# Kernel tuning notes

Measured on AMD Instinct MI355X. Metric: run time of the kernel, lower is better.

## Reference

```python
import jax, jax.numpy as jnp
import numpy as np

N_LAYER = 4
N_HEAD = 8
N_EMBD = 512
HEAD_SIZE = N_EMBD // N_HEAD
VOCAB = 32000
BLOCK = 2048
WINDOW = 64
N_GLOBAL = 16
N_RANDOM = 16
B = 2
T = 2048


def setup_inputs() -> dict:
    key = jax.random.key(0)
    ks = jax.random.split(key, 24)
    s = 0.02
    inp = {
        "tok_emb": jax.random.normal(ks[0], (VOCAB, N_EMBD), jnp.float32) * s,
        "pos_emb": jax.random.normal(ks[1], (BLOCK, N_EMBD), jnp.float32) * s,
        "Wq": jax.random.normal(ks[2], (N_LAYER, N_HEAD, N_EMBD, HEAD_SIZE), jnp.float32) * s,
        "Wk": jax.random.normal(ks[3], (N_LAYER, N_HEAD, N_EMBD, HEAD_SIZE), jnp.float32) * s,
        "Wv": jax.random.normal(ks[4], (N_LAYER, N_HEAD, N_EMBD, HEAD_SIZE), jnp.float32) * s,
        "Wproj": jax.random.normal(ks[5], (N_LAYER, N_EMBD, N_EMBD), jnp.float32) * s,
        "bproj": jnp.zeros((N_LAYER, N_EMBD), jnp.float32),
        "ln1_g": jnp.ones((N_LAYER, N_EMBD), jnp.float32),
        "ln1_b": jnp.zeros((N_LAYER, N_EMBD), jnp.float32),
        "ln2_g": jnp.ones((N_LAYER, N_EMBD), jnp.float32),
        "ln2_b": jnp.zeros((N_LAYER, N_EMBD), jnp.float32),
        "W1": jax.random.normal(ks[6], (N_LAYER, N_EMBD, 4 * N_EMBD), jnp.float32) * s,
        "b1": jnp.zeros((N_LAYER, 4 * N_EMBD), jnp.float32),
        "W2": jax.random.normal(ks[7], (N_LAYER, 4 * N_EMBD, N_EMBD), jnp.float32) * s,
        "b2": jnp.zeros((N_LAYER, N_EMBD), jnp.float32),
        "lnf_g": jnp.ones((N_EMBD,), jnp.float32),
        "lnf_b": jnp.zeros((N_EMBD,), jnp.float32),
        "Wout": jax.random.normal(ks[8], (N_EMBD, VOCAB), jnp.float32) * s,
        "bout": jnp.zeros((VOCAB,), jnp.float32),
        "input_tokens": jax.random.randint(ks[9], (B, T), 0, VOCAB, jnp.int32),
        "random_cols": jax.random.randint(ks[10], (N_LAYER, N_HEAD, T, N_RANDOM), 0, T, jnp.int32),
    }
    return inp


def _layernorm(x, g, b):
    mu = jnp.mean(x, axis=-1, keepdims=True)
    var = jnp.var(x, axis=-1, keepdims=True)
    return (x - mu) * jax.lax.rsqrt(var + 1e-5) * g + b


def _static_masks(t):
    rows = jnp.arange(t)[:, None]
    cols = jnp.arange(t)[None, :]
    causal = rows >= cols
    local = (cols >= rows - WINDOW + 1) & (cols <= rows)
    glob = (rows < N_GLOBAL) | (cols < N_GLOBAL)
    return local | glob, causal  # base [T,T], causal [T,T]


def _random_mask(rc):  # rc: [H, T, R] -> [H, T, T] bool
    h, t, r = rc.shape
    m = jnp.zeros((h, t, t), dtype=bool)
    hi = jnp.arange(h)[:, None, None]
    ri = jnp.arange(t)[None, :, None]
    return m.at[hi, ri, rc].set(True)


def _forward(tok_emb, pos_emb, Wq, Wk, Wv, Wproj, bproj, ln1_g, ln1_b, ln2_g, ln2_b,
             W1, b1, W2, b2, lnf_g, lnf_b, Wout, bout, input_tokens, random_cols):
    b, t = input_tokens.shape
    x = tok_emb[input_tokens] + pos_emb[:t]  # [B,T,C]
    base, causal = _static_masks(t)
    scale = HEAD_SIZE ** -0.5
    neg_inf = jnp.finfo(x.dtype).min
    for l in range(N_LAYER):
        xn = _layernorm(x, ln1_g[l], ln1_b[l])
        q = jnp.einsum('btc,hcd->bhtd', xn, Wq[l])
        k = jnp.einsum('btc,hcd->bhtd', xn, Wk[l])
        v = jnp.einsum('btc,hcd->bhtd', xn, Wv[l])
        w = jnp.einsum('bhtd,bhsd->bhts', q, k) * scale  # [B,H,T,T]
        final = (base[None] | _random_mask(random_cols[l])) & causal[None]  # [H,T,T]
        w = jnp.where(final[None], w, neg_inf)
        w = jax.nn.softmax(w, axis=-1)
        attn = jnp.einsum('bhts,bhsd->bhtd', w, v)  # [B,H,T,hs]
        attn = attn.transpose(0, 2, 1, 3).reshape(b, t, N_EMBD)
        x = x + attn @ Wproj[l] + bproj[l]
        xn = _layernorm(x, ln2_g[l], ln2_b[l])
        h = jax.nn.relu(xn @ W1[l] + b1[l])
        x = x + h @ W2[l] + b2[l]
    x = _layernorm(x, lnf_g, lnf_b)
    return x @ Wout + bout  # logits [B,T,V]


def reference(tok_emb, pos_emb, Wq, Wk, Wv, Wproj, bproj, ln1_g, ln1_b, ln2_g, ln2_b,
              W1, b1, W2, b2, lnf_g, lnf_b, Wout, bout, input_tokens, random_cols):
    return _forward(tok_emb, pos_emb, Wq, Wk, Wv, Wproj, bproj, ln1_g, ln1_b, ln2_g, ln2_b,
                    W1, b1, W2, b2, lnf_g, lnf_b, Wout, bout, input_tokens, random_cols)
```

## Files before the change

kernel.cpp:

```cpp
#include <hip/hip_runtime.h>
#include <hip/hip_bf16.h>

#define NLAYER 4
#define NHEAD 8
#define CEMB 512
#define HS 64
#define VOCAB_N 32000
#define SEQT 2048
#define BATCH_N 2
#define MROWS (BATCH_N * SEQT)
#define WIN 64
#define NGLOB 16
#define NRAND 16
#define QB 16

typedef __attribute__((ext_vector_type(8))) __bf16 bf16x8;
typedef __attribute__((ext_vector_type(4))) float f32x4;
typedef __attribute__((ext_vector_type(8))) unsigned short u16x8;

__device__ __forceinline__ unsigned short f2bf(float f) {
    unsigned u = __float_as_uint(f);
    u += 0x7fffu + ((u >> 16) & 1u);
    return (unsigned short)(u >> 16);
}
__device__ __forceinline__ float bf2f(unsigned short v) {
    return __uint_as_float((unsigned)v << 16);
}

__device__ __forceinline__ void stage16(const unsigned short* g, unsigned short* l) {
    __builtin_amdgcn_global_load_lds(
        (const __attribute__((address_space(1))) void*)g,
        (__attribute__((address_space(3))) void*)l, 16, 0, 0);
}

__global__ __launch_bounds__(256) void transpose_all_kernel(
    const float* __restrict__ Wq, const float* __restrict__ Wk,
    const float* __restrict__ Wv, const float* __restrict__ Wproj,
    const float* __restrict__ W1, const float* __restrict__ W2,
    const float* __restrict__ Wout,
    unsigned short* __restrict__ wqkvT, unsigned short* __restrict__ wprojT,
    unsigned short* __restrict__ w1T, unsigned short* __restrict__ w2T,
    unsigned short* __restrict__ woutT)
{
    __shared__ float tle[64][65];
    const int bid = blockIdx.x;
    const float* src; unsigned short* dst; int Ks, Ns, k0, n0;
    if (bid < 768) {
        const int tile = bid & 7, rest = bid >> 3;
        const int l = rest / 24, r2 = rest % 24;
        const int sel = r2 >> 3, h = r2 & 7;
        const float* W = (sel == 0) ? Wq : (sel == 1) ? Wk : Wv;
        src = W + (size_t)(l * 8 + h) * 512 * 64;
        dst = wqkvT + ((size_t)l * 1536 + sel * 512 + h * 64) * 512;
        Ks = 512; Ns = 64; k0 = tile * 64; n0 = 0;
    } else if (bid < 1024) {
        const int idx = bid - 768, l = idx >> 6, t6 = idx & 63;
        src = Wproj + (size_t)l * 512 * 512;
        dst = wprojT + (size_t)l * 512 * 512;
        Ks = 512; Ns = 512; k0 = (t6 >> 3) * 64; n0 = (t6 & 7) * 64;
    } else if (bid < 2048) {
        const int idx = bid - 1024, l = idx >> 8, t8 = idx & 255;
        src = W1 + (size_t)l * 512 * 2048;
        dst = w1T + (size_t)l * 2048 * 512;
        Ks = 512; Ns = 2048; k0 = (t8 >> 5) * 64; n0 = (t8 & 31) * 64;
    } else if (bid < 3072) {
        const int idx = bid - 2048, l = idx >> 8, t8 = idx & 255;
        src = W2 + (size_t)l * 2048 * 512;
        dst = w2T + (size_t)l * 512 * 2048;
        Ks = 2048; Ns = 512; k0 = (t8 >> 3) * 64; n0 = (t8 & 7) * 64;
    } else {
        const int idx = bid - 3072;
        src = Wout; dst = woutT;
        Ks = 512; Ns = 32000; k0 = (idx / 500) * 64; n0 = (idx % 500) * 64;
    }
    const int tid = threadIdx.x;
    #pragma unroll
    for (int i = 0; i < 16; ++i) {
        const int idx = tid + i * 256;
        const int r = idx >> 6, c = idx & 63;
        tle[r][c] = src[(size_t)(k0 + r) * Ns + n0 + c];
    }
    __syncthreads();
    #pragma unroll
    for (int i = 0; i < 16; ++i) {
        const int idx = tid + i * 256;
        const int c = idx >> 6, r = idx & 63;
        dst[(size_t)(n0 + c) * Ks + k0 + r] = f2bf(tle[r][c]);
    }
}

__global__ __launch_bounds__(256) void embed_kernel(
    const float* __restrict__ tok_emb, const float* __restrict__ pos_emb,
    const int* __restrict__ toks, float* __restrict__ x)
{
    int i = blockIdx.x * 256 + threadIdx.x;
    int m = i >> 7;
    int c = (i & 127) << 2;
    int tok = toks[m];
    const float4 a = *(const float4*)&tok_emb[(size_t)tok * CEMB + c];
    const float4 p = *(const float4*)&pos_emb[(size_t)(m & (SEQT - 1)) * CEMB + c];
    float4 o;
    o.x = a.x + p.x; o.y = a.y + p.y; o.z = a.z + p.z; o.w = a.w + p.w;
    *(float4*)&x[(size_t)m * CEMB + c] = o;
}

__global__ __launch_bounds__(256) void ln_kernel(
    const float* __restrict__ x, const float* __restrict__ g,
    const float* __restrict__ b, unsigned short* __restrict__ out)
{
    const int wave = threadIdx.x >> 6, lane = threadIdx.x & 63;
    const int m = blockIdx.x * 4 + wave;
    const float* row = x + (size_t)m * CEMB;
    const float4 v0 = *(const float4*)&row[lane * 8];
    const float4 v1 = *(const float4*)&row[lane * 8 + 4];
    float s  = v0.x + v0.y + v0.z + v0.w + v1.x + v1.y + v1.z + v1.w;
    float s2 = v0.x*v0.x + v0.y*v0.y + v0.z*v0.z + v0.w*v0.w
             + v1.x*v1.x + v1.y*v1.y + v1.z*v1.z + v1.w*v1.w;
    #pragma unroll
    for (int off = 32; off > 0; off >>= 1) {
        s  += __shfl_xor(s, off);
        s2 += __shfl_xor(s2, off);
    }
    const float mu  = s * (1.f / CEMB);
    const float var = s2 * (1.f / CEMB) - mu * mu;
    const float rs  = rsqrtf(var + 1e-5f);
    const float vals[8] = {v0.x, v0.y, v0.z, v0.w, v1.x, v1.y, v1.z, v1.w};
    u16x8 o;
    #pragma unroll
    for (int j = 0; j < 8; ++j)
        o[j] = f2bf((vals[j] - mu) * rs * g[lane * 8 + j] + b[lane * 8 + j]);
    *(u16x8*)&out[(size_t)m * CEMB + lane * 8] = o;
}

template<int MODE, int NF, int SWZ>
__global__ __launch_bounds__(256) void gemm_kernel(
    const unsigned short* __restrict__ A, const unsigned short* __restrict__ Bt,
    const float* __restrict__ bias, const float* resid, void* outp,
    int M, int N, int K)
{
    __shared__ unsigned short sa[2][128 * 32];
    __shared__ unsigned short sb[2][NF * 32 * 32];
    const int tid = threadIdx.x;
    const int lane = tid & 63;
    const int wave = tid >> 6;
    const int wr = wave >> 1, wc = wave & 1;

    int bx = blockIdx.x, by = blockIdx.y;
    if (SWZ == 2) {
        const int flat = by * gridDim.x + bx;
        const int q = (gridDim.x * gridDim.y) >> 3;
        const int nl = (flat & 7) * q + (flat >> 3);
        by = nl & 31;
        bx = nl >> 5;
    }
    const int m0 = by * 128;
    const int n0 = bx * (NF * 32);

    const int c0a = (wave * 2) * 64 + lane;
    const int c1a = (wave * 2 + 1) * 64 + lane;
    const int r0 = c0a >> 2, kk0 = (c0a & 3) * 8;
    const int r1 = c1a >> 2, kk1 = (c1a & 3) * 8;
    const unsigned short* ga0 = A + (size_t)(m0 + r0) * K + kk0;
    const unsigned short* ga1 = A + (size_t)(m0 + r1) * K + kk1;
    const int o0 = (wave * 2) * 512;
    const int o1 = (wave * 2 + 1) * 512;
    const int cb0 = (NF == 4) ? c0a : wave * 64 + lane;
    const int cb1 = c1a;
    const int rb0 = cb0 >> 2, kb0 = (cb0 & 3) * 8;
    const int rb1 = cb1 >> 2, kb1 = (cb1 & 3) * 8;
    const unsigned short* gb0 = Bt + (size_t)(n0 + rb0) * K + kb0;
    const unsigned short* gb1 = Bt + (size_t)(n0 + rb1) * K + kb1;
    const int ob0 = (NF == 4) ? o0 : wave * 512;
    const int ob1 = o1;

    f32x4 acc[4][NF] = {};
    const int kro = (lane >> 4) * 8;
    const int fr = lane & 15;

    stage16(ga0, &sa[0][o0]);
    stage16(ga1, &sa[0][o1]);
    stage16(gb0, &sb[0][ob0]);
    if (NF == 4) stage16(gb1, &sb[0][ob1]);
    __syncthreads();

    const int nt = K >> 5;
    int cur = 0;
    for (int t = 0; t < nt; ++t) {
        if (t + 1 < nt) {
            const int k1 = (t + 1) << 5;
            stage16(ga0 + k1, &sa[cur ^ 1][o0]);
            stage16(ga1 + k1, &sa[cur ^ 1][o1]);
            stage16(gb0 + k1, &sb[cur ^ 1][ob0]);
            if (NF == 4) stage16(gb1 + k1, &sb[cur ^ 1][ob1]);
        }
        bf16x8 af[4], bfr[NF];
        #pragma unroll
        for (int i = 0; i < 4; ++i)
            af[i] = *reinterpret_cast<const bf16x8*>(&sa[cur][(wr * 64 + i * 16 + fr) * 32 + kro]);
        #pragma unroll
        for (int i = 0; i < NF; ++i)
            bfr[i] = *reinterpret_cast<const bf16x8*>(&sb[cur][(wc * (NF * 16) + i * 16 + fr) * 32 + kro]);
        #pragma unroll
        for (int mi = 0; mi < 4; ++mi)
            #pragma unroll
            for (int ni = 0; ni < NF; ++ni)
                acc[mi][ni] = __builtin_amdgcn_mfma_f32_16x16x32_bf16(af[mi], bfr[ni], acc[mi][ni], 0, 0, 0);
        __syncthreads();
        cur ^= 1;
    }

    #pragma unroll
    for (int mi = 0; mi < 4; ++mi) {
        #pragma unroll
        for (int ni = 0; ni < NF; ++ni) {
            const int gc = n0 + wc * (NF * 16) + ni * 16 + fr;
            const float bv = (MODE != 0) ? bias[gc] : 0.f;
            #pragma unroll
            for (int r = 0; r < 4; ++r) {
                const int gr = m0 + wr * 64 + mi * 16 + (lane >> 4) * 4 + r;
                float v = acc[mi][ni][r] + bv;
                if (MODE == 1) v += resid[(size_t)gr * N + gc];
                if (MODE == 2) v = fmaxf(v, 0.f);
                if (MODE == 0 || MODE == 2) {
                    ((unsigned short*)outp)[(size_t)gr * N + gc] = f2bf(v);
                } else {
                    ((float*)outp)[(size_t)gr * N + gc] = v;
                }
            }
        }
    }
}

__global__ __launch_bounds__(256) void attn_kernel(
    const unsigned short* __restrict__ qkv, const int* __restrict__ rc,
    unsigned short* __restrict__ attnout)
{
    __shared__ unsigned short Kw[80 * 64];
    __shared__ unsigned short Vw[80 * 64];
    __shared__ float ewA[4][64];
    __shared__ float cwW[4][40];
    __shared__ int   cwC[4][40];

    const int tid = threadIdx.x;
    const int wave = tid >> 6, lane = tid & 63;
    const int bid = blockIdx.x;
    const int tb = bid & 127;
    const int h = (bid >> 7) & 7;
    const int b = bid >> 10;
    const int t0 = tb * QB;
    const int base = t0 - 63;

    const unsigned short* kb = qkv + (size_t)b * SEQT * 1536 + 512 + h * 64;
    const unsigned short* vb = qkv + (size_t)b * SEQT * 1536 + 1024 + h * 64;

    for (int c = tid; c < 79 * 8; c += 256) {
        const int r = c >> 3, j = c & 7;
        const int col = base + r;
        u16x8 kv = {0, 0, 0, 0, 0, 0, 0, 0};
        u16x8 vv = {0, 0, 0, 0, 0, 0, 0, 0};
        if (col >= 0) {
            kv = *(const u16x8*)&kb[(size_t)col * 1536 + j * 8];
            vv = *(const u16x8*)&vb[(size_t)col * 1536 + j * 8];
        }
        *(u16x8*)&Kw[r * 64 + ((j ^ (r & 7)) * 8)] = kv;
        *(u16x8*)&Vw[r * 64 + j * 8] = vv;
    }
    __syncthreads();

    for (int u = 0; u < 4; ++u) {
        const int Q = wave * 4 + u;
        const int t = t0 + Q;
        const int m = b * SEQT + t;

        u16x8 qreg[8];
        #pragma unroll
        for (int j = 0; j < 8; ++j)
            qreg[j] = *(const u16x8*)&qkv[(size_t)m * 1536 + h * 64 + j * 8];

        const int row = Q + lane;
        const int colA = base + row;
        float sA;
        {
            float s = 0.f;
            #pragma unroll
            for (int j = 0; j < 8; ++j) {
                const u16x8 kc = *(const u16x8*)&Kw[row * 64 + ((j ^ (row & 7)) * 8)];
                #pragma unroll
                for (int e = 0; e < 8; ++e)
                    s += bf2f(kc[e]) * bf2f(qreg[j][e]);
            }
            sA = (colA >= NGLOB) ? s * 0.125f : -1e30f;
        }

        int colB = 0;
        bool vB = false;
        if (lane < NGLOB) {
            colB = lane;
            vB = (lane <= t);
        } else if (lane < 32) {
            colB = rc[((size_t)h * SEQT + t) * NRAND + (lane - 16)];
            vB = (colB >= NGLOB) && (colB <= t - WIN);
        }
        #pragma unroll
        for (int j = 0; j < 15; ++j) {
            const int cj = __shfl(colB, 16 + j);
            if (lane >= 16 && lane < 32 && (lane - 16) > j && cj == colB) vB = false;
        }

        float sB = -1e30f;
        if (vB) {
            float s = 0.f;
            const unsigned short* kr = &kb[(size_t)colB * 1536];
            #pragma unroll
            for (int j = 0; j < 8; ++j) {
                const u16x8 kc = *(const u16x8*)&kr[j * 8];
                #pragma unroll
                for (int e = 0; e < 8; ++e)
                    s += bf2f(kc[e]) * bf2f(qreg[j][e]);
            }
            sB = s * 0.125f;
        }

        float mx = fmaxf(sA, sB);
        #pragma unroll
        for (int off = 32; off > 0; off >>= 1) mx = fmaxf(mx, __shfl_xor(mx, off));
        const float e0 = (colA >= NGLOB) ? __expf(sA - mx) : 0.f;
        const float e1 = vB ? __expf(sB - mx) : 0.f;
        float sum = e0 + e1;
        #pragma unroll
        for (int off = 32; off > 0; off >>= 1) sum += __shfl_xor(sum, off);
        const float inv = 1.f / sum;

        ewA[wave][lane] = e0;
        const unsigned long long bm = __ballot(vB);
        const int nB = __popcll(bm);
        const int pos = __popcll(bm & ((1ull << lane) - 1ull));
        if (vB) { cwC[wave][pos] = colB; cwW[wave][pos] = e1; }
        if (lane >= 32 && lane < 36) {
            const int p = nB + (lane - 32);
            cwC[wave][p] = 0; cwW[wave][p] = 0.f;
        }

        float acc = 0.f;
        #pragma unroll 8
        for (int s = 0; s < 64; ++s)
            acc += ewA[wave][s] * bf2f(Vw[(Q + s) * 64 + lane]);

        const int nB4 = (nB + 3) & ~3;
        for (int i = 0; i < nB4; i += 4) {
            const float w0 = cwW[wave][i + 0], w1 = cwW[wave][i + 1];
            const float w2 = cwW[wave][i + 2], w3 = cwW[wave][i + 3];
            const int   c0 = cwC[wave][i + 0], c1 = cwC[wave][i + 1];
            const int   c2 = cwC[wave][i + 2], c3 = cwC[wave][i + 3];
            const float x0 = bf2f(vb[(size_t)c0 * 1536 + lane]);
            const float x1 = bf2f(vb[(size_t)c1 * 1536 + lane]);
            const float x2 = bf2f(vb[(size_t)c2 * 1536 + lane]);
            const float x3 = bf2f(vb[(size_t)c3 * 1536 + lane]);
            acc += w0 * x0 + w1 * x1 + w2 * x2 + w3 * x3;
        }

        attnout[(size_t)m * CEMB + h * 64 + lane] = f2bf(acc * inv);
    }
}

extern "C" void kernel_launch(void* const* d_in, const int* in_sizes, int n_in,
                              void* d_out, int out_size, void* d_ws, size_t ws_size,
                              hipStream_t stream)
{
    const float* tok_emb = (const float*)d_in[0];
    const float* pos_emb = (const float*)d_in[1];
    const float* Wq    = (const float*)d_in[2];
    const float* Wk    = (const float*)d_in[3];
    const float* Wv    = (const float*)d_in[4];
    const float* Wproj = (const float*)d_in[5];
    const float* bproj = (const float*)d_in[6];
    const float* ln1g  = (const float*)d_in[7];
    const float* ln1b  = (const float*)d_in[8];
    const float* ln2g  = (const float*)d_in[9];
    const float* ln2b  = (const float*)d_in[10];
    const float* W1    = (const float*)d_in[11];
    const float* b1    = (const float*)d_in[12];
    const float* W2    = (const float*)d_in[13];
    const float* b2    = (const float*)d_in[14];
    const float* lnfg  = (const float*)d_in[15];
    const float* lnfb  = (const float*)d_in[16];
    const float* Wout  = (const float*)d_in[17];
    const float* bout  = (const float*)d_in[18];
    const int*   toks  = (const int*)d_in[19];
    const int*   rcols = (const int*)d_in[20];
    (void)in_sizes; (void)n_in; (void)out_size; (void)ws_size;

    char* ws = (char*)d_ws;
    size_t off = 0;
    auto ALLOC = [&](size_t bytes) -> void* {
        void* p = ws + off;
        off += (bytes + 255) & ~(size_t)255;
        return p;
    };
    float*          x      = (float*)ALLOC((size_t)MROWS * CEMB * 4);
    unsigned short* xnbf   = (unsigned short*)ALLOC((size_t)MROWS * CEMB * 2);
    unsigned short* qkv    = (unsigned short*)ALLOC((size_t)MROWS * 1536 * 2);
    unsigned short* attnbf = (unsigned short*)ALLOC((size_t)MROWS * CEMB * 2);
    unsigned short* hbf    = (unsigned short*)ALLOC((size_t)MROWS * 2048 * 2);
    unsigned short* wqkvT  = (unsigned short*)ALLOC((size_t)NLAYER * 1536 * 512 * 2);
    unsigned short* wprojT = (unsigned short*)ALLOC((size_t)NLAYER * 512 * 512 * 2);
    unsigned short* w1T    = (unsigned short*)ALLOC((size_t)NLAYER * 2048 * 512 * 2);
    unsigned short* w2T    = (unsigned short*)ALLOC((size_t)NLAYER * 512 * 2048 * 2);
    unsigned short* woutT  = (unsigned short*)ALLOC((size_t)VOCAB_N * 512 * 2);

    transpose_all_kernel<<<7072, 256, 0, stream>>>(
        Wq, Wk, Wv, Wproj, W1, W2, Wout, wqkvT, wprojT, w1T, w2T, woutT);

    embed_kernel<<<2048, 256, 0, stream>>>(tok_emb, pos_emb, toks, x);

    for (int l = 0; l < NLAYER; ++l) {
        ln_kernel<<<1024, 256, 0, stream>>>(x, ln1g + l * CEMB, ln1b + l * CEMB, xnbf);
        gemm_kernel<0, 2, 0><<<dim3(24, 32), 256, 0, stream>>>(
            xnbf, wqkvT + (size_t)l * 1536 * 512, nullptr, nullptr, qkv, MROWS, 1536, 512);
        attn_kernel<<<2048, 256, 0, stream>>>(qkv, rcols + (size_t)l * NHEAD * SEQT * NRAND, attnbf);
        gemm_kernel<1, 2, 0><<<dim3(8, 32), 256, 0, stream>>>(
            attnbf, wprojT + (size_t)l * 512 * 512, bproj + l * CEMB, x, x, MROWS, 512, 512);
        ln_kernel<<<1024, 256, 0, stream>>>(x, ln2g + l * CEMB, ln2b + l * CEMB, xnbf);
        gemm_kernel<2, 4, 0><<<dim3(16, 32), 256, 0, stream>>>(
            xnbf, w1T + (size_t)l * 2048 * 512, b1 + l * 2048, nullptr, hbf, MROWS, 2048, 512);
        gemm_kernel<1, 2, 0><<<dim3(8, 32), 256, 0, stream>>>(
            hbf, w2T + (size_t)l * 512 * 2048, b2 + l * CEMB, x, x, MROWS, 512, 2048);
    }
    ln_kernel<<<1024, 256, 0, stream>>>(x, lnfg, lnfb, xnbf);
    gemm_kernel<3, 4, 2><<<dim3(250, 32), 256, 0, stream>>>(
        xnbf, woutT, bout, nullptr, d_out, MROWS, VOCAB_N, 512);
}
```

Baseline: 1.037 ms.

## Triple-buffer GEMM shared-memory staging with explicit vmcnt waits

New measurement: 1.035 ms. About the same (-0.2%).

```diff
diff --git a/kernel.cpp b/kernel.cpp
--- a/kernel.cpp
+++ b/kernel.cpp
@@ -138,8 +138,8 @@
     const float* __restrict__ bias, const float* resid, void* outp,
     int M, int N, int K)
 {
-    __shared__ unsigned short sa[2][128 * 32];
-    __shared__ unsigned short sb[2][NF * 32 * 32];
+    __shared__ unsigned short sa[3][128 * 32];
+    __shared__ unsigned short sb[3][NF * 32 * 32];
     const int tid = threadIdx.x;
     const int lane = tid & 63;
     const int wave = tid >> 6;
@@ -177,22 +177,34 @@
     const int kro = (lane >> 4) * 8;
     const int fr = lane & 15;
 
-    stage16(ga0, &sa[0][o0]);
-    stage16(ga1, &sa[0][o1]);
-    stage16(gb0, &sb[0][ob0]);
-    if (NF == 4) stage16(gb1, &sb[0][ob1]);
-    __syncthreads();
+    auto STAGE = [&](int tile, int buf) {
+        const int kk = tile << 5;
+        stage16(ga0 + kk, &sa[buf][o0]);
+        stage16(ga1 + kk, &sa[buf][o1]);
+        stage16(gb0 + kk, &sb[buf][ob0]);
+        if constexpr (NF == 4) stage16(gb1 + kk, &sb[buf][ob1]);
+    };
 
     const int nt = K >> 5;
+    STAGE(0, 0);
+    STAGE(1, 1);
+
     int cur = 0;
     for (int t = 0; t < nt; ++t) {
         if (t + 1 < nt) {
-            const int k1 = (t + 1) << 5;
-            stage16(ga0 + k1, &sa[cur ^ 1][o0]);
-            stage16(ga1 + k1, &sa[cur ^ 1][o1]);
-            stage16(gb0 + k1, &sb[cur ^ 1][ob0]);
-            if (NF == 4) stage16(gb1 + k1, &sb[cur ^ 1][ob1]);
-        }
+            if constexpr (NF == 2) asm volatile("s_waitcnt vmcnt(3)" ::: "memory");
+            else                   asm volatile("s_waitcnt vmcnt(4)" ::: "memory");
+        } else {
+            asm volatile("s_waitcnt vmcnt(0)" ::: "memory");
+        }
+        __builtin_amdgcn_s_barrier();
+        __builtin_amdgcn_sched_barrier(0);
+
+        if (t + 2 < nt) {
+            int b2 = cur + 2; if (b2 >= 3) b2 -= 3;
+            STAGE(t + 2, b2);
+        }
+
         bf16x8 af[4], bfr[NF];
         #pragma unroll
         for (int i = 0; i < 4; ++i)
@@ -205,8 +217,8 @@
             #pragma unroll
             for (int ni = 0; ni < NF; ++ni)
                 acc[mi][ni] = __builtin_amdgcn_mfma_f32_16x16x32_bf16(af[mi], bfr[ni], acc[mi][ni], 0, 0, 0);
-        __syncthreads();
-        cur ^= 1;
+
+        cur = (cur == 2) ? 0 : cur + 1;
     }
 
     #pragma unroll
```
